# Kernel tuning notes

Hardware: AMD Instinct MI355X
Metric: run time of the kernel (lower is better)

Reference implementation:

```python
import jax, jax.numpy as jnp
from jax import lax
import numpy as np


def setup_inputs() -> dict:
    key = jax.random.key(0)
    ks = jax.random.split(key, 5)
    B = 256
    data = jax.random.normal(ks[0], (B, 1, 28, 28), jnp.float32)
    # ConvLayer: Conv2d(1->256, k=9, s=1)
    w1 = jax.random.normal(ks[1], (256, 1, 9, 9), jnp.float32) * 0.1
    b1 = jnp.zeros((256,), jnp.float32)
    # PrimaryCaps: Conv2d(256->256, k=9, s=2)
    w2 = jax.random.normal(ks[2], (256, 256, 9, 9), jnp.float32) * 0.02
    b2 = jnp.zeros((256,), jnp.float32)
    # DigitCaps routing weights: (in_caps=1152, out_caps=10, out_len=16, in_len=8)
    W = jax.random.normal(ks[3], (1152, 10, 16, 8), jnp.float32) * 0.05
    return {"data": data, "w1": w1, "b1": b1, "w2": w2, "b2": b2, "W": W}


def _squash(s):
    # s: (B,1,10,16); sn*s / ((1+sn)*sqrt(sn)) as in the torch code
    sn = jnp.sum(s * s, axis=-1, keepdims=True)
    return sn * s / ((1.0 + sn) * jnp.sqrt(sn))


def reference(data, w1, b1, w2, b2, W):
    # ConvLayer: conv k9 s1 VALID + relu -> (B,256,20,20)
    x = lax.conv(data, w1, (1, 1), 'VALID') + b1[None, :, None, None]
    x = jax.nn.relu(x)
    # PrimaryCaps: conv k9 s2 VALID -> (B,256,6,6)
    x = lax.conv(x, w2, (2, 2), 'VALID') + b2[None, :, None, None]
    B = x.shape[0]
    # toCapsules: (B,256,6,6) -> (B,8,32,6,6) -> (B,8,1152) -> (B,1152,8)
    x = x.reshape(B, 8, -1).transpose(0, 2, 1)
    # u_hat[b,n,o,k] = W[n,o,k,d] @ x[b,n,d]  -> (B,1152,10,16)
    u_hat = jnp.einsum('nokd,bnd->bnok', W, x)
    b_ij = jnp.zeros((B, 1152, 10, 1), u_hat.dtype)
    num_iterations = 3
    v_j = None
    for it in range(1, num_iterations + 1):
        c_ij = jax.nn.softmax(b_ij, axis=1)            # over input capsules
        s_j = jnp.sum(c_ij * u_hat, axis=1, keepdims=True)  # (B,1,10,16)
        v_j = _squash(s_j)
        if it < num_iterations:
            # Faithful to the torch code: a_ij = u_hat * sum_k(v_j), broadcast
            # over input capsules; b_ij widens to (B,1152,10,16) after iter 1.
            a_ij = u_hat * jnp.sum(v_j, axis=-1, keepdims=True)
            b_ij = b_ij + a_ij
    return v_j[:, 0]  # (B,10,16)
```

## Files before the change

### kernel.cpp

```cpp
#include <hip/hip_runtime.h>
#include <hip/hip_bf16.h>
#include <cmath>


typedef float f32x4 __attribute__((ext_vector_type(4)));
typedef short s16x8 __attribute__((ext_vector_type(8)));
typedef unsigned int u32;

static __device__ __forceinline__ short f2bf(float x) {
  __hip_bfloat16 h = __float2bfloat16(x);
  return *reinterpret_cast<short*>(&h);
}
static __device__ __forceinline__ float bf2f(short s) {
  __hip_bfloat16 h;
  *reinterpret_cast<short*>(&h) = s;
  return __bfloat162float(h);
}
static __device__ __forceinline__ void stage16(const short* g, short* l) {
  __builtin_amdgcn_global_load_lds(
      (const __attribute__((address_space(1))) u32*)(const void*)g,
      (__attribute__((address_space(3))) u32*)(void*)l, 16, 0, 0);
}

#define CHUNK_SHORTS 23552
#define ODD_OFS 12288

__global__ __launch_bounds__(256) void prep_all(
    const float* __restrict__ w2, s16x8* __restrict__ wstg,
    const float* __restrict__ data, const float* __restrict__ w1,
    const float* __restrict__ b1, short* __restrict__ c1g) {
  __shared__ float sbuf[10368];
  const int t = threadIdx.x;
  if (blockIdx.x < 512) {
    const int b = blockIdx.x;
    const int chunk = b >> 6;
    const int kg = (b >> 4) & 3;
    const int cot = b & 15;
    const int co0 = cot * 16;
    const size_t gbase = (size_t)(chunk * 32 + kg * 8) * 81;
    for (int i = t; i < 10368; i += 256) {
      const int r = i / 648, e = i - r * 648;
      sbuf[i] = w2[(size_t)(co0 + r) * 20736 + gbase + e];
    }
    __syncthreads();
    for (int p = t; p < 1296; p += 256) {
      const int tap = p >> 4, co = p & 15;
      s16x8 hi, lo;
#pragma unroll
      for (int i = 0; i < 8; ++i) {
        const float x = sbuf[co * 648 + i * 81 + tap];
        const short h = f2bf(x);
        hi[i] = h;
        lo[i] = f2bf(x - bf2f(h));
      }
      const size_t T = (size_t)(chunk * 81 + tap);
      wstg[T * 2048 + kg * 256 + co0 + co] = hi;
      wstg[T * 2048 + 1024 + kg * 256 + co0 + co] = lo;
    }
    return;
  }
  const int cb = blockIdx.x - 512;
  const int img = cb >> 1;
  const int yh = cb & 1;
  float* simg = sbuf;
  for (int i = t; i < 19 * 28; i += 256) {
    const int r = i / 28, c = i % 28;
    if (yh * 10 + r < 28) simg[r * 36 + c] = data[img * 784 + (yh * 10 + r) * 28 + c];
  }
  __syncthreads();
  for (int task = t; task < 2560; task += 256) {
    const int ci = task & 255;
    const int yl = task >> 8;
    const int y = yh * 10 + yl;
    if (y >= 19) continue;
    const float* wr = w1 + ci * 81;
    float acc[20];
    const float bz = b1[ci];
#pragma unroll
    for (int x = 0; x < 20; ++x) acc[x] = bz;
#pragma unroll
    for (int ky = 0; ky < 9; ++ky) {
      float rr[28];
#pragma unroll
      for (int q = 0; q < 7; ++q)
        *(float4*)&rr[q * 4] = *(const float4*)&simg[(yl + ky) * 36 + q * 4];
#pragma unroll
      for (int kx = 0; kx < 9; ++kx) {
        const float w = wr[ky * 9 + kx];
#pragma unroll
        for (int x = 0; x < 20; ++x) acc[x] = fmaf(w, rr[x + kx], acc[x]);
      }
    }
    const int chunk = ci >> 5, cil = ci & 31, kg = cil >> 3, il = cil & 7;
    short* cbase = c1g + (size_t)(img * 8 + chunk) * CHUNK_SHORTS;
#pragma unroll
    for (int x = 0; x < 19; ++x) {
      const int xh = x >> 1;
      const int r = (x & 1) ? (y * 9 + xh) : (y * 10 + xh);
      short* base = cbase + ((x & 1) ? ODD_OFS : 0);
      const float v = fmaxf(acc[x], 0.f);
      const short hi = f2bf(v);
      const short lo = f2bf(v - bf2f(hi));
      base[r * 64 + (((kg + r) & 7) << 3) + il] = hi;
      base[r * 64 + (((kg + 4 + r) & 7) << 3) + il] = lo;
    }
  }
}

__global__ __launch_bounds__(256) void conv2_mfma(
    const short* __restrict__ c1g, const short* __restrict__ wstg,
    const float* __restrict__ b2, float* __restrict__ xcaps0,
    float* __restrict__ xcaps1) {
  const int t = threadIdx.x;
  const int bid = blockIdx.x;
  const int xcd = bid & 7;
  const int ksp = xcd & 1;
  const int coh = (xcd >> 1) & 1;
  const int img = (bid >> 3) * 2 + (xcd >> 2);
  const int lane = t & 63;
  const int wv = t >> 6;
  const int r16 = lane & 15;
  const int kg = lane >> 4;

  __shared__ short c1[12288];

  int arowE[3], arowO[3];
#pragma unroll
  for (int m = 0; m < 3; ++m) {
    int pos = m * 16 + r16;
    if (pos > 35) pos = 35;
    const int oy = pos / 6, ox = pos % 6;
    arowE[m] = oy * 20 + ox;
    arowO[m] = oy * 18 + ox;
  }
  int bOff[2], con[2];
  float bias[2];
#pragma unroll
  for (int j = 0; j < 2; ++j) {
    const int co = coh * 128 + wv * 32 + j * 16 + r16;
    con[j] = co;
    bOff[j] = kg * 256 + co;
    bias[j] = (ksp == 0) ? b2[co] : 0.f;
  }
  float* xcp = (ksp == 0) ? xcaps0 : xcaps1;

  const f32x4 vzero = {0.f, 0.f, 0.f, 0.f};
  f32x4 acc[3][2];
#pragma unroll
  for (int m = 0; m < 3; ++m)
#pragma unroll
    for (int j = 0; j < 2; ++j) acc[m][j] = vzero;

  const s16x8* wsv = (const s16x8*)wstg;

  for (int cc = 0; cc < 4; ++cc) {
    const int chunk = ksp * 4 + cc;
    const short* src = c1g + (size_t)(img * 8 + chunk) * CHUNK_SHORTS;
    const size_t bb = (size_t)chunk * 81 * 2048;

    __syncthreads();
    for (int c = wv; c < 24; c += 4)
      stage16(src + c * 512 + lane * 8, &c1[c * 512]);
    __syncthreads();
    {
      s16x8 BHc[2], BLc[2];
#pragma unroll
      for (int j = 0; j < 2; ++j) {
        BHc[j] = wsv[bb + bOff[j]];
        BLc[j] = wsv[bb + bOff[j] + 1024];
      }
      for (int ky = 0; ky < 9; ++ky) {
#pragma unroll
        for (int kxi = 0; kxi < 5; ++kxi) {
          s16x8 BHn[2], BLn[2];
          if (!(ky == 8 && kxi == 4)) {
            const int nky = (kxi == 4) ? ky + 1 : ky;
            const int nkxi = (kxi == 4) ? 0 : kxi + 1;
            const size_t nb = bb + (size_t)(nky * 9 + 2 * nkxi) * 2048;
#pragma unroll
            for (int j = 0; j < 2; ++j) {
              BHn[j] = wsv[nb + bOff[j]];
              BLn[j] = wsv[nb + bOff[j] + 1024];
            }
          }
          s16x8 AH[3], AL[3];
#pragma unroll
          for (int m = 0; m < 3; ++m) {
            const int r = arowE[m] + ky * 10 + kxi;
            AH[m] = *(const s16x8*)&c1[r * 64 + (((kg + r) & 7) << 3)];
            AL[m] = *(const s16x8*)&c1[r * 64 + (((kg + 4 + r) & 7) << 3)];
          }
#pragma unroll
          for (int m = 0; m < 3; ++m)
#pragma unroll
            for (int j = 0; j < 2; ++j)
              acc[m][j] = __builtin_amdgcn_mfma_f32_16x16x32_bf16(AH[m], BHc[j], acc[m][j], 0, 0, 0);
#pragma unroll
          for (int m = 0; m < 3; ++m)
#pragma unroll
            for (int j = 0; j < 2; ++j)
              acc[m][j] = __builtin_amdgcn_mfma_f32_16x16x32_bf16(AL[m], BHc[j], acc[m][j], 0, 0, 0);
#pragma unroll
          for (int m = 0; m < 3; ++m)
#pragma unroll
            for (int j = 0; j < 2; ++j)
              acc[m][j] = __builtin_amdgcn_mfma_f32_16x16x32_bf16(AH[m], BLc[j], acc[m][j], 0, 0, 0);
#pragma unroll
          for (int j = 0; j < 2; ++j) { BHc[j] = BHn[j]; BLc[j] = BLn[j]; }
        }
      }
    }

    __syncthreads();
    for (int c = wv; c < 22; c += 4)
      stage16(src + ODD_OFS + c * 512 + lane * 8, &c1[c * 512]);
    __syncthreads();
    {
      s16x8 BHc[2], BLc[2];
#pragma unroll
      for (int j = 0; j < 2; ++j) {
        BHc[j] = wsv[bb + 2048 + bOff[j]];
        BLc[j] = wsv[bb + 2048 + bOff[j] + 1024];
      }
      for (int ky = 0; ky < 9; ++ky) {
#pragma unroll
        for (int kxi = 0; kxi < 4; ++kxi) {
          s16x8 BHn[2], BLn[2];
          if (!(ky == 8 && kxi == 3)) {
            const int nky = (kxi == 3) ? ky + 1 : ky;
            const int nkxi = (kxi == 3) ? 0 : kxi + 1;
            const size_t nb = bb + (size_t)(nky * 9 + 2 * nkxi + 1) * 2048;
#pragma unroll
            for (int j = 0; j < 2; ++j) {
              BHn[j] = wsv[nb + bOff[j]];
              BLn[j] = wsv[nb + bOff[j] + 1024];
            }
          }
          s16x8 AH[3], AL[3];
#pragma unroll
          for (int m = 0; m < 3; ++m) {
            const int r = arowO[m] + ky * 9 + kxi;
            AH[m] = *(const s16x8*)&c1[r * 64 + (((kg + r) & 7) << 3)];
            AL[m] = *(const s16x8*)&c1[r * 64 + (((kg + 4 + r) & 7) << 3)];
          }
#pragma unroll
          for (int m = 0; m < 3; ++m)
#pragma unroll
            for (int j = 0; j < 2; ++j)
              acc[m][j] = __builtin_amdgcn_mfma_f32_16x16x32_bf16(AH[m], BHc[j], acc[m][j], 0, 0, 0);
#pragma unroll
          for (int m = 0; m < 3; ++m)
#pragma unroll
            for (int j = 0; j < 2; ++j)
              acc[m][j] = __builtin_amdgcn_mfma_f32_16x16x32_bf16(AL[m], BHc[j], acc[m][j], 0, 0, 0);
#pragma unroll
          for (int m = 0; m < 3; ++m)
#pragma unroll
            for (int j = 0; j < 2; ++j)
              acc[m][j] = __builtin_amdgcn_mfma_f32_16x16x32_bf16(AH[m], BLc[j], acc[m][j], 0, 0, 0);
#pragma unroll
          for (int j = 0; j < 2; ++j) { BHc[j] = BHn[j]; BLc[j] = BLn[j]; }
        }
      }
    }
  }

#pragma unroll
  for (int m = 0; m < 3; ++m) {
#pragma unroll
    for (int jj = 0; jj < 4; ++jj) {
      const int pos = m * 16 + kg * 4 + jj;
      if (pos < 36) {
#pragma unroll
        for (int j = 0; j < 2; ++j) {
          const int co = con[j];
          const int n = (co & 31) * 36 + pos;
          xcp[((size_t)img * 1152 + n) * 8 + (co >> 5)] = acc[m][j][jj] + bias[j];
        }
      }
    }
  }
}

__global__ __launch_bounds__(256) void routing_fused(const float* __restrict__ xcaps0,
                                                     const float* __restrict__ xcaps1,
                                                     const float* __restrict__ W,
                                                     float* __restrict__ out) {
  const int o = blockIdx.x >> 7;
  const int bp = blockIdx.x & 127;
  const int b0 = bp * 2, b1 = b0 + 1;
  const int t = threadIdx.x;
  const int k = t & 15, ng = t >> 4;
  __shared__ float xs0[1152 * 8];
  __shared__ float xs1[1152 * 8];
  __shared__ double redA[256], redB[256], redC[256], redD[256];
  __shared__ float s0s[16], s1s[16];
  __shared__ float sv0, sv1;
  __shared__ double f0, f1;

  {
    const float4* p00 = (const float4*)(xcaps0 + (size_t)b0 * 9216);
    const float4* p01 = (const float4*)(xcaps1 + (size_t)b0 * 9216);
    const float4* p10 = (const float4*)(xcaps0 + (size_t)b1 * 9216);
    const float4* p11 = (const float4*)(xcaps1 + (size_t)b1 * 9216);
    float4* d0 = (float4*)xs0;
    float4* d1 = (float4*)xs1;
    for (int i = t; i < 2304; i += 256) {
      float4 a = p00[i], b = p01[i];
      float4 c = p10[i], d = p11[i];
      float4 s0, s1;
      s0.x = a.x + b.x; s0.y = a.y + b.y; s0.z = a.z + b.z; s0.w = a.w + b.w;
      s1.x = c.x + d.x; s1.y = c.y + d.y; s1.z = c.z + d.z; s1.w = c.w + d.w;
      d0[i] = s0;
      d1[i] = s1;
    }
  }
  __syncthreads();

  const int n0 = ng * 72;
  float u0[72], u1[72];
  const float* wp = W + ((size_t)(n0 * 10 + o) * 16 + k) * 8;
#pragma unroll
  for (int i = 0; i < 72; ++i) {
    const float* wq = wp + (size_t)i * 1280;
    const float4 wa = *(const float4*)wq;
    const float4 wb = *(const float4*)(wq + 4);
    const float4 xa0 = *(const float4*)&xs0[(n0 + i) * 8];
    const float4 xb0 = *(const float4*)&xs0[(n0 + i) * 8 + 4];
    const float4 xa1 = *(const float4*)&xs1[(n0 + i) * 8];
    const float4 xb1 = *(const float4*)&xs1[(n0 + i) * 8 + 4];
    float s0 = wa.x * xa0.x + wa.y * xa0.y + wa.z * xa0.z + wa.w * xa0.w
             + wb.x * xb0.x + wb.y * xb0.y + wb.z * xb0.z + wb.w * xb0.w;
    float s1 = wa.x * xa1.x + wa.y * xa1.y + wa.z * xa1.z + wa.w * xa1.w
             + wb.x * xb1.x + wb.y * xb1.y + wb.z * xb1.z + wb.w * xb1.w;
    u0[i] = s0;
    u1[i] = s1;
  }

  {
    double S0 = 0.0, S1 = 0.0;
#pragma unroll
    for (int i = 0; i < 72; ++i) { S0 += (double)u0[i]; S1 += (double)u1[i]; }
    redA[t] = S0; redB[t] = S1;
  }
  __syncthreads();
  if (t < 16) {
    double t0 = 0.0, t1 = 0.0;
#pragma unroll
    for (int g = 0; g < 16; ++g) { t0 += redA[g * 16 + t]; t1 += redB[g * 16 + t]; }
    s0s[t] = (float)(t0 * (double)(1.0f / 1152.0f));
    s1s[t] = (float)(t1 * (double)(1.0f / 1152.0f));
  }
  __syncthreads();
  if (t == 0) {
    double sn = 0.0;
#pragma unroll
    for (int kk = 0; kk < 16; ++kk) sn += (double)s0s[kk] * (double)s0s[kk];
    double f = sn / ((1.0 + sn) * sqrt(sn));
    double sv = 0.0;
#pragma unroll
    for (int kk = 0; kk < 16; ++kk) sv += (double)s0s[kk] * f;
    sv0 = (float)sv;
    sn = 0.0;
#pragma unroll
    for (int kk = 0; kk < 16; ++kk) sn += (double)s1s[kk] * (double)s1s[kk];
    f = sn / ((1.0 + sn) * sqrt(sn));
    sv = 0.0;
#pragma unroll
    for (int kk = 0; kk < 16; ++kk) sv += (double)s1s[kk] * f;
    sv1 = (float)sv;
  }
  __syncthreads();
  const float v10 = sv0, v11 = sv1;

  {
    double E0 = 0.0, EU0 = 0.0, E1 = 0.0, EU1 = 0.0;
#pragma unroll
    for (int i = 0; i < 72; ++i) {
      const float e0 = expf(u0[i] * v10);
      E0 += (double)e0;
      EU0 += (double)e0 * (double)u0[i];
      const float e1 = expf(u1[i] * v11);
      E1 += (double)e1;
      EU1 += (double)e1 * (double)u1[i];
    }
    redA[t] = E0; redB[t] = EU0; redC[t] = E1; redD[t] = EU1;
  }
  __syncthreads();
  if (t < 16) {
    double e0 = 0.0, s0 = 0.0, e1 = 0.0, s1 = 0.0;
#pragma unroll
    for (int g = 0; g < 16; ++g) {
      e0 += redA[g * 16 + t]; s0 += redB[g * 16 + t];
      e1 += redC[g * 16 + t]; s1 += redD[g * 16 + t];
    }
    s0s[t] = (float)(s0 / e0);
    s1s[t] = (float)(s1 / e1);
  }
  __syncthreads();
  if (t == 0) {
    double sn = 0.0;
#pragma unroll
    for (int kk = 0; kk < 16; ++kk) sn += (double)s0s[kk] * (double)s0s[kk];
    double f = sn / ((1.0 + sn) * sqrt(sn));
    double sv = 0.0;
#pragma unroll
    for (int kk = 0; kk < 16; ++kk) sv += (double)s0s[kk] * f;
    sv0 = v10 + (float)sv;
    sn = 0.0;
#pragma unroll
    for (int kk = 0; kk < 16; ++kk) sn += (double)s1s[kk] * (double)s1s[kk];
    f = sn / ((1.0 + sn) * sqrt(sn));
    sv = 0.0;
#pragma unroll
    for (int kk = 0; kk < 16; ++kk) sv += (double)s1s[kk] * f;
    sv1 = v11 + (float)sv;
  }
  __syncthreads();
  const float v20 = sv0, v21 = sv1;

  {
    double E0 = 0.0, EU0 = 0.0, E1 = 0.0, EU1 = 0.0;
#pragma unroll
    for (int i = 0; i < 72; ++i) {
      const float e0 = expf(u0[i] * v20);
      E0 += (double)e0;
      EU0 += (double)e0 * (double)u0[i];
      const float e1 = expf(u1[i] * v21);
      E1 += (double)e1;
      EU1 += (double)e1 * (double)u1[i];
    }
    redA[t] = E0; redB[t] = EU0; redC[t] = E1; redD[t] = EU1;
  }
  __syncthreads();
  if (t < 16) {
    double e0 = 0.0, s0 = 0.0, e1 = 0.0, s1 = 0.0;
#pragma unroll
    for (int g = 0; g < 16; ++g) {
      e0 += redA[g * 16 + t]; s0 += redB[g * 16 + t];
      e1 += redC[g * 16 + t]; s1 += redD[g * 16 + t];
    }
    s0s[t] = (float)(s0 / e0);
    s1s[t] = (float)(s1 / e1);
  }
  __syncthreads();
  if (t == 0) {
    double sn = 0.0;
#pragma unroll
    for (int kk = 0; kk < 16; ++kk) sn += (double)s0s[kk] * (double)s0s[kk];
    f0 = sn / ((1.0 + sn) * sqrt(sn));
    sn = 0.0;
#pragma unroll
    for (int kk = 0; kk < 16; ++kk) sn += (double)s1s[kk] * (double)s1s[kk];
    f1 = sn / ((1.0 + sn) * sqrt(sn));
  }
  __syncthreads();
  if (t < 16) {
    out[b0 * 160 + o * 16 + t] = (float)((double)s0s[t] * f0);
    out[b1 * 160 + o * 16 + t] = (float)((double)s1s[t] * f1);
  }
}

extern "C" void kernel_launch(void* const* d_in, const int* in_sizes, int n_in,
                              void* d_out, int out_size, void* d_ws, size_t ws_size,
                              hipStream_t stream) {
  const float* data = (const float*)d_in[0];
  const float* w1   = (const float*)d_in[1];
  const float* b1   = (const float*)d_in[2];
  const float* w2   = (const float*)d_in[3];
  const float* b2   = (const float*)d_in[4];
  const float* W    = (const float*)d_in[5];
  float* out = (float*)d_out;

  short* wstg   = (short*)d_ws;
  short* c1g    = wstg + 10616832;
  float* xcaps0 = (float*)(c1g + 48234496);
  float* xcaps1 = xcaps0 + 2359296;

  prep_all<<<1024, 256, 0, stream>>>(w2, (s16x8*)wstg, data, w1, b1, c1g);
  conv2_mfma<<<1024, 256, 0, stream>>>(c1g, wstg, b2, xcaps0, xcaps1);
  routing_fused<<<1280, 256, 0, stream>>>(xcaps0, xcaps1, W, out);
}
```

Baseline: 531.7 us.

## Process one image per routing block with padded LDS and wave-shuffle reductions

The routing kernel now handles a single image per block instead of two, launching twice as many blocks. This halves the per-thread register arrays and the LDS footprint, and the x tile is stored with a stride of 9 floats to reduce bank conflicts. The cross-thread sums now use wave shuffles followed by a small four-wave LDS reduction instead of a 256-entry double array. The cost is that each W row is loaded twice as often in total, since it is no longer shared between two images, and the dot products now read scalar LDS values instead of float4 loads.

```diff
diff --git a/kernel.cpp b/kernel.cpp
--- a/kernel.cpp
+++ b/kernel.cpp
@@ -286,179 +286,142 @@
                                                      const float* __restrict__ xcaps1,
                                                      const float* __restrict__ W,
                                                      float* __restrict__ out) {
-  const int o = blockIdx.x >> 7;
-  const int bp = blockIdx.x & 127;
-  const int b0 = bp * 2, b1 = b0 + 1;
+  const int o = blockIdx.x >> 8;
+  const int b = blockIdx.x & 255;
   const int t = threadIdx.x;
   const int k = t & 15, ng = t >> 4;
-  __shared__ float xs0[1152 * 8];
-  __shared__ float xs1[1152 * 8];
-  __shared__ double redA[256], redB[256], redC[256], redD[256];
-  __shared__ float s0s[16], s1s[16];
-  __shared__ float sv0, sv1;
-  __shared__ double f0, f1;
+  const int wavei = t >> 6, lane = t & 63;
+  __shared__ float xs[1152 * 9];
+  __shared__ double sredA[4][16];
+  __shared__ double sredB[4][16];
+  __shared__ float s_s[16];
+  __shared__ float s_sv;
+  __shared__ double s_f;
 
   {
-    const float4* p00 = (const float4*)(xcaps0 + (size_t)b0 * 9216);
-    const float4* p01 = (const float4*)(xcaps1 + (size_t)b0 * 9216);
-    const float4* p10 = (const float4*)(xcaps0 + (size_t)b1 * 9216);
-    const float4* p11 = (const float4*)(xcaps1 + (size_t)b1 * 9216);
-    float4* d0 = (float4*)xs0;
-    float4* d1 = (float4*)xs1;
-    for (int i = t; i < 2304; i += 256) {
-      float4 a = p00[i], b = p01[i];
-      float4 c = p10[i], d = p11[i];
-      float4 s0, s1;
-      s0.x = a.x + b.x; s0.y = a.y + b.y; s0.z = a.z + b.z; s0.w = a.w + b.w;
-      s1.x = c.x + d.x; s1.y = c.y + d.y; s1.z = c.z + d.z; s1.w = c.w + d.w;
-      d0[i] = s0;
-      d1[i] = s1;
+    const float4* p0 = (const float4*)(xcaps0 + (size_t)b * 9216);
+    const float4* p1 = (const float4*)(xcaps1 + (size_t)b * 9216);
+    for (int idx = t; idx < 2304; idx += 256) {
+      float4 a = p0[idx];
+      const float4 c = p1[idx];
+      a.x += c.x; a.y += c.y; a.z += c.z; a.w += c.w;
+      const int n = idx >> 1, h = idx & 1;
+      float* dst = &xs[n * 9 + h * 4];
+      dst[0] = a.x; dst[1] = a.y; dst[2] = a.z; dst[3] = a.w;
     }
   }
   __syncthreads();
 
   const int n0 = ng * 72;
-  float u0[72], u1[72];
+  float u[72];
   const float* wp = W + ((size_t)(n0 * 10 + o) * 16 + k) * 8;
 #pragma unroll
   for (int i = 0; i < 72; ++i) {
     const float* wq = wp + (size_t)i * 1280;
     const float4 wa = *(const float4*)wq;
     const float4 wb = *(const float4*)(wq + 4);
-    const float4 xa0 = *(const float4*)&xs0[(n0 + i) * 8];
-    const float4 xb0 = *(const float4*)&xs0[(n0 + i) * 8 + 4];
-    const float4 xa1 = *(const float4*)&xs1[(n0 + i) * 8];
-    const float4 xb1 = *(const float4*)&xs1[(n0 + i) * 8 + 4];
-    float s0 = wa.x * xa0.x + wa.y * xa0.y + wa.z * xa0.z + wa.w * xa0.w
-             + wb.x * xb0.x + wb.y * xb0.y + wb.z * xb0.z + wb.w * xb0.w;
-    float s1 = wa.x * xa1.x + wa.y * xa1.y + wa.z * xa1.z + wa.w * xa1.w
-             + wb.x * xb1.x + wb.y * xb1.y + wb.z * xb1.z + wb.w * xb1.w;
-    u0[i] = s0;
-    u1[i] = s1;
+    const float* xp = &xs[(n0 + i) * 9];
+    float s = fmaf(wa.x, xp[0], 0.f);
+    s = fmaf(wa.y, xp[1], s);
+    s = fmaf(wa.z, xp[2], s);
+    s = fmaf(wa.w, xp[3], s);
+    s = fmaf(wb.x, xp[4], s);
+    s = fmaf(wb.y, xp[5], s);
+    s = fmaf(wb.z, xp[6], s);
+    s = fmaf(wb.w, xp[7], s);
+    u[i] = s;
   }
 
   {
-    double S0 = 0.0, S1 = 0.0;
-#pragma unroll
-    for (int i = 0; i < 72; ++i) { S0 += (double)u0[i]; S1 += (double)u1[i]; }
-    redA[t] = S0; redB[t] = S1;
+    double S = 0.0;
+#pragma unroll
+    for (int i = 0; i < 72; ++i) S += (double)u[i];
+    S += __shfl_xor(S, 16);
+    S += __shfl_xor(S, 32);
+    if (lane < 16) sredA[wavei][lane] = S;
   }
   __syncthreads();
   if (t < 16) {
-    double t0 = 0.0, t1 = 0.0;
-#pragma unroll
-    for (int g = 0; g < 16; ++g) { t0 += redA[g * 16 + t]; t1 += redB[g * 16 + t]; }
-    s0s[t] = (float)(t0 * (double)(1.0f / 1152.0f));
-    s1s[t] = (float)(t1 * (double)(1.0f / 1152.0f));
+    const double tot = sredA[0][t] + sredA[1][t] + sredA[2][t] + sredA[3][t];
+    s_s[t] = (float)(tot * (double)(1.0f / 1152.0f));
   }
   __syncthreads();
   if (t == 0) {
     double sn = 0.0;
 #pragma unroll
-    for (int kk = 0; kk < 16; ++kk) sn += (double)s0s[kk] * (double)s0s[kk];
-    double f = sn / ((1.0 + sn) * sqrt(sn));
+    for (int kk = 0; kk < 16; ++kk) sn += (double)s_s[kk] * (double)s_s[kk];
+    const double f = sn / ((1.0 + sn) * sqrt(sn));
     double sv = 0.0;
 #pragma unroll
-    for (int kk = 0; kk < 16; ++kk) sv += (double)s0s[kk] * f;
-    sv0 = (float)sv;
-    sn = 0.0;
-#pragma unroll
-    for (int kk = 0; kk < 16; ++kk) sn += (double)s1s[kk] * (double)s1s[kk];
-    f = sn / ((1.0 + sn) * sqrt(sn));
-    sv = 0.0;
-#pragma unroll
-    for (int kk = 0; kk < 16; ++kk) sv += (double)s1s[kk] * f;
-    sv1 = (float)sv;
-  }
-  __syncthreads();
-  const float v10 = sv0, v11 = sv1;
+    for (int kk = 0; kk < 16; ++kk) sv += (double)s_s[kk] * f;
+    s_sv = (float)sv;
+  }
+  __syncthreads();
+  const float sv1 = s_sv;
 
   {
-    double E0 = 0.0, EU0 = 0.0, E1 = 0.0, EU1 = 0.0;
+    double E = 0.0, EU = 0.0;
 #pragma unroll
     for (int i = 0; i < 72; ++i) {
-      const float e0 = expf(u0[i] * v10);
-      E0 += (double)e0;
-      EU0 += (double)e0 * (double)u0[i];
-      const float e1 = expf(u1[i] * v11);
-      E1 += (double)e1;
-      EU1 += (double)e1 * (double)u1[i];
-    }
-    redA[t] = E0; redB[t] = EU0; redC[t] = E1; redD[t] = EU1;
+      const float e = expf(u[i] * sv1);
+      E += (double)e;
+      EU += (double)e * (double)u[i];
+    }
+    E += __shfl_xor(E, 16);
+    E += __shfl_xor(E, 32);
+    EU += __shfl_xor(EU, 16);
+    EU += __shfl_xor(EU, 32);
+    if (lane < 16) { sredA[wavei][lane] = E; sredB[wavei][lane] = EU; }
   }
   __syncthreads();
   if (t < 16) {
-    double e0 = 0.0, s0 = 0.0, e1 = 0.0, s1 = 0.0;
-#pragma unroll
-    for (int g = 0; g < 16; ++g) {
-      e0 += redA[g * 16 + t]; s0 += redB[g * 16 + t];
-      e1 += redC[g * 16 + t]; s1 += redD[g * 16 + t];
-    }
-    s0s[t] = (float)(s0 / e0);
-    s1s[t] = (float)(s1 / e1);
+    const double te = sredA[0][t] + sredA[1][t] + sredA[2][t] + sredA[3][t];
+    const double tu = sredB[0][t] + sredB[1][t] + sredB[2][t] + sredB[3][t];
+    s_s[t] = (float)(tu / te);
   }
   __syncthreads();
   if (t == 0) {
     double sn = 0.0;
 #pragma unroll
-    for (int kk = 0; kk < 16; ++kk) sn += (double)s0s[kk] * (double)s0s[kk];
-    double f = sn / ((1.0 + sn) * sqrt(sn));
+    for (int kk = 0; kk < 16; ++kk) sn += (double)s_s[kk] * (double)s_s[kk];
+    const double f = sn / ((1.0 + sn) * sqrt(sn));
     double sv = 0.0;
 #pragma unroll
-    for (int kk = 0; kk < 16; ++kk) sv += (double)s0s[kk] * f;
-    sv0 = v10 + (float)sv;
-    sn = 0.0;
-#pragma unroll
-    for (int kk = 0; kk < 16; ++kk) sn += (double)s1s[kk] * (double)s1s[kk];
-    f = sn / ((1.0 + sn) * sqrt(sn));
-    sv = 0.0;
-#pragma unroll
-    for (int kk = 0; kk < 16; ++kk) sv += (double)s1s[kk] * f;
-    sv1 = v11 + (float)sv;
-  }
-  __syncthreads();
-  const float v20 = sv0, v21 = sv1;
+    for (int kk = 0; kk < 16; ++kk) sv += (double)s_s[kk] * f;
+    s_sv = sv1 + (float)sv;
+  }
+  __syncthreads();
+  const float sv12 = s_sv;
 
   {
-    double E0 = 0.0, EU0 = 0.0, E1 = 0.0, EU1 = 0.0;
+    double E = 0.0, EU = 0.0;
 #pragma unroll
     for (int i = 0; i < 72; ++i) {
-      const float e0 = expf(u0[i] * v20);
-      E0 += (double)e0;
-      EU0 += (double)e0 * (double)u0[i];
-      const float e1 = expf(u1[i] * v21);
-      E1 += (double)e1;
-      EU1 += (double)e1 * (double)u1[i];
-    }
-    redA[t] = E0; redB[t] = EU0; redC[t] = E1; redD[t] = EU1;
+      const float e = expf(u[i] * sv12);
+      E += (double)e;
+      EU += (double)e * (double)u[i];
+    }
+    E += __shfl_xor(E, 16);
+    E += __shfl_xor(E, 32);
+    EU += __shfl_xor(EU, 16);
+    EU += __shfl_xor(EU, 32);
+    if (lane < 16) { sredA[wavei][lane] = E; sredB[wavei][lane] = EU; }
   }
   __syncthreads();
   if (t < 16) {
-    double e0 = 0.0, s0 = 0.0, e1 = 0.0, s1 = 0.0;
-#pragma unroll
-    for (int g = 0; g < 16; ++g) {
-      e0 += redA[g * 16 + t]; s0 += redB[g * 16 + t];
-      e1 += redC[g * 16 + t]; s1 += redD[g * 16 + t];
-    }
-    s0s[t] = (float)(s0 / e0);
-    s1s[t] = (float)(s1 / e1);
+    const double te = sredA[0][t] + sredA[1][t] + sredA[2][t] + sredA[3][t];
+    const double tu = sredB[0][t] + sredB[1][t] + sredB[2][t] + sredB[3][t];
+    s_s[t] = (float)(tu / te);
   }
   __syncthreads();
   if (t == 0) {
     double sn = 0.0;
 #pragma unroll
-    for (int kk = 0; kk < 16; ++kk) sn += (double)s0s[kk] * (double)s0s[kk];
-    f0 = sn / ((1.0 + sn) * sqrt(sn));
-    sn = 0.0;
-#pragma unroll
-    for (int kk = 0; kk < 16; ++kk) sn += (double)s1s[kk] * (double)s1s[kk];
-    f1 = sn / ((1.0 + sn) * sqrt(sn));
-  }
-  __syncthreads();
-  if (t < 16) {
-    out[b0 * 160 + o * 16 + t] = (float)((double)s0s[t] * f0);
-    out[b1 * 160 + o * 16 + t] = (float)((double)s1s[t] * f1);
-  }
+    for (int kk = 0; kk < 16; ++kk) sn += (double)s_s[kk] * (double)s_s[kk];
+    s_f = sn / ((1.0 + sn) * sqrt(sn));
+  }
+  __syncthreads();
+  if (t < 16) out[b * 160 + o * 16 + t] = (float)((double)s_s[t] * s_f);
 }
 
 extern "C" void kernel_launch(void* const* d_in, const int* in_sizes, int n_in,
@@ -479,5 +442,5 @@
 
   prep_all<<<1024, 256, 0, stream>>>(w2, (s16x8*)wstg, data, w1, b1, c1g);
   conv2_mfma<<<1024, 256, 0, stream>>>(c1g, wstg, b2, xcaps0, xcaps1);
-  routing_fused<<<1280, 256, 0, stream>>>(xcaps0, xcaps1, W, out);
-}
+  routing_fused<<<2560, 256, 0, stream>>>(xcaps0, xcaps1, W, out);
+}
```

New measurement: 555.9 us. +4.6%, slower.
